# Kernel tuning notes

Measured on AMD Instinct MI355X. Metric: run time of the kernel, lower is better.

Reference implementation:

```python
import jax, jax.numpy as jnp
import numpy as np

N_NODES = 100000
N_EDGES = 3200000
N_GRAPHS = 2000
F_IN, H, N_CLS = 14, 64, 2


def _glorot(key, shape):
    lim = float(np.sqrt(6.0 / (shape[0] + shape[1])))
    return jax.random.uniform(key, shape, jnp.float32, -lim, lim)


def setup_inputs() -> dict:
    key = jax.random.key(0)
    ks = jax.random.split(key, 16)
    x = jax.random.normal(ks[0], (N_NODES, F_IN), jnp.float32)
    edge_index = jax.random.randint(ks[1], (2, N_EDGES), 0, N_NODES, jnp.int64)
    batch = jnp.sort(jax.random.randint(ks[2], (N_NODES,), 0, N_GRAPHS, jnp.int64))
    return {
        "x": x,
        "W1l": _glorot(ks[3], (F_IN, H)), "W1r": _glorot(ks[4], (F_IN, H)), "b1": jnp.zeros((H,), jnp.float32),
        "W2l": _glorot(ks[5], (H, H)), "W2r": _glorot(ks[6], (H, H)), "b2": jnp.zeros((H,), jnp.float32),
        "W3l": _glorot(ks[7], (H, H)), "W3r": _glorot(ks[8], (H, H)), "b3": jnp.zeros((H,), jnp.float32),
        "W4l": _glorot(ks[9], (H, N_CLS)), "W4r": _glorot(ks[10], (H, N_CLS)), "b4": jnp.zeros((N_CLS,), jnp.float32),
        "edge_index": edge_index,
        "batch": batch,
    }


def _sage_conv(x, Wl, Wr, b, src, dst, inv_deg):
    # mean-aggregate neighbor features: messages flow src -> dst (PyG SAGEConv default)
    agg = jax.ops.segment_sum(x[src], dst, num_segments=N_NODES) * inv_deg
    return agg @ Wl + x @ Wr + b


def reference(x, W1l, W1r, b1, W2l, W2r, b2, W3l, W3r, b3, W4l, W4r, b4, edge_index, batch):
    src, dst = edge_index[0], edge_index[1]
    ones = jnp.ones((src.shape[0],), x.dtype)
    deg = jax.ops.segment_sum(ones, dst, num_segments=N_NODES)
    inv_deg = (1.0 / jnp.maximum(deg, 1.0))[:, None]  # [N,1], isolated nodes -> 0 agg

    h = jax.nn.relu(_sage_conv(x, W1l, W1r, b1, src, dst, inv_deg))
    h = jax.nn.relu(_sage_conv(h, W2l, W2r, b2, src, dst, inv_deg))
    h = jax.nn.relu(_sage_conv(h, W3l, W3r, b3, src, dst, inv_deg))
    h = _sage_conv(h, W4l, W4r, b4, src, dst, inv_deg)

    # global_mean_pool over graphs
    gsum = jax.ops.segment_sum(h, batch, num_segments=N_GRAPHS)
    gcnt = jax.ops.segment_sum(jnp.ones((h.shape[0],), h.dtype), batch, num_segments=N_GRAPHS)
    pooled = gsum / jnp.maximum(gcnt, 1.0)[:, None]
    return jax.nn.log_softmax(pooled, axis=-1)
```

## Files before the change

### kernel.cpp

```cpp
#include <hip/hip_runtime.h>
#include <hip/hip_fp16.h>

#define NN 100000
#define NE 3200000
#define NG 2000
#define FIN 14
#define HD 64
#define NC 2

#define NBUK 256
#define BNODES 391
#define P1E 4096
#define BUFCAP 13312

#define AHU 68
#define WCH 136
#define NGB ((NN + 63) / 64)

typedef unsigned int uint;
typedef short short8 __attribute__((ext_vector_type(8)));
typedef float f32x4 __attribute__((ext_vector_type(4)));
union U128 { uint4 u; short8 s; };

__device__ __forceinline__ __half2 u2h(uint u) {
    union { uint u; __half2 h; } c; c.u = u; return c.h;
}
__device__ __forceinline__ uint h2u(__half2 h) {
    union { __half2 h; uint u; } c; c.h = h; return c.u;
}
__device__ __forceinline__ uint pkh(float a, float b) {
    return h2u(__floats2half2_rn(a, b));
}
__device__ __forceinline__ uint pack2bf16(float a, float b) {
    uint ua = __float_as_uint(a), ub = __float_as_uint(b);
    ua = (ua + 0x7FFFu + ((ua >> 16) & 1u)) >> 16;
    ub = (ub + 0x7FFFu + ((ub >> 16) & 1u)) >> 16;
    return ua | (ub << 16);
}
__device__ __forceinline__ unsigned short bf16of(float a) {
    uint ua = __float_as_uint(a);
    return (unsigned short)((ua + 0x7FFFu + ((ua >> 16) & 1u)) >> 16);
}


__global__ __launch_bounds__(256) void k_hist_bucket(const int* __restrict__ dst,
                                                     int* __restrict__ bkcnt) {
    __shared__ int cnt[NBUK];
    int t = threadIdx.x;
    cnt[t] = 0;
    __syncthreads();
    int e0 = blockIdx.x * P1E;
    int m = NE - e0; if (m > P1E) m = P1E;
    for (int e = t; e < m; e += 256) atomicAdd(&cnt[dst[e0 + e] / BNODES], 1);
    __syncthreads();
    if (cnt[t] > 0) atomicAdd(&bkcnt[t], cnt[t]);
}

__global__ void k_scanb(const int* __restrict__ bkcnt, int* __restrict__ bbase,
                        int* __restrict__ bcur) {
    __shared__ int tmp[NBUK];
    int t = threadIdx.x;
    int v = bkcnt[t];
    tmp[t] = v;
    __syncthreads();
    for (int off = 1; off < NBUK; off <<= 1) {
        int u = (t >= off) ? tmp[t - off] : 0;
        __syncthreads();
        tmp[t] += u;
        __syncthreads();
    }
    int excl = tmp[t] - v;
    bbase[t] = excl;
    bcur[t] = excl;
    if (t == NBUK - 1) bbase[NBUK] = tmp[t];
}

__global__ void k_gbounds(const int* __restrict__ batch, int* __restrict__ gstart,
                          int* __restrict__ gend) {
    int i = blockIdx.x * blockDim.x + threadIdx.x;
    if (i < NN) {
        int b = batch[i];
        if (i == 0 || batch[i - 1] != b) gstart[b] = i;
        if (i == NN - 1 || batch[i + 1] != b) gend[b] = i + 1;
    }
}

__global__ __launch_bounds__(256) void k_pass1(
    const int* __restrict__ src, const int* __restrict__ dst,
    int* __restrict__ bcur, int* __restrict__ pairs) {
    __shared__ int cnt[NBUK];
    __shared__ int scanb[NBUK + 1];
    __shared__ int cur[NBUK];
    __shared__ int gbase[NBUK];
    __shared__ int pbuf[P1E];
    __shared__ unsigned char bsl[P1E];
    int t = threadIdx.x;
    int e0 = blockIdx.x * P1E;
    int m = NE - e0; if (m > P1E) m = P1E;
    cnt[t] = 0;
    __syncthreads();
    int ds[16], ss[16], bk[16];
#pragma unroll
    for (int j = 0; j < 16; ++j) {
        int e = t + j * 256;
        if (e < m) {
            ds[j] = dst[e0 + e];
            ss[j] = src[e0 + e];
            bk[j] = ds[j] / BNODES;
            atomicAdd(&cnt[bk[j]], 1);
        } else bk[j] = -1;
    }
    __syncthreads();
    int v = cnt[t];
    scanb[t] = v;
    __syncthreads();
    for (int off = 1; off < 256; off <<= 1) {
        int u = (t >= off) ? scanb[t - off] : 0;
        __syncthreads();
        scanb[t] += u;
        __syncthreads();
    }
    int excl = scanb[t] - v;
    scanb[t] = excl;
    cur[t] = excl;
    if (t == 255) scanb[256] = excl + v;
    __syncthreads();
#pragma unroll
    for (int j = 0; j < 16; ++j) {
        if (bk[j] >= 0) {
            int p = atomicAdd(&cur[bk[j]], 1);
            pbuf[p] = ss[j] | ((ds[j] - bk[j] * BNODES) << 17);
            bsl[p] = (unsigned char)bk[j];
        }
    }
    int cb = scanb[t + 1] - scanb[t];
    if (cb > 0) gbase[t] = atomicAdd(&bcur[t], cb);
    __syncthreads();
    for (int s = t; s < m; s += 256) {
        int b = bsl[s];
        pairs[gbase[b] + (s - scanb[b])] = pbuf[s];
    }
}

__global__ __launch_bounds__(256) void k_pass2(
    const int* __restrict__ pairs, const int* __restrict__ bbase,
    int* __restrict__ deg, int* __restrict__ rs, int* __restrict__ csr) {
    __shared__ int buf1[BUFCAP];
    __shared__ int buf2[BUFCAP];
    __shared__ int cnt[512];
    __shared__ int rsl[512];
    __shared__ int cur[512];
    __shared__ int s1[256];
    int b = blockIdx.x;
    int n0 = b * BNODES;
    if (n0 >= NN) return;
    int nlocal = NN - n0; if (nlocal > BNODES) nlocal = BNODES;
    int t = threadIdx.x;
    int base = bbase[b];
    int m = bbase[b + 1] - base;
    bool fits = (m <= BUFCAP);
    cnt[t] = 0; cnt[t + 256] = 0;
    __syncthreads();
    for (int s = t; s < m; s += 256) {
        int pk = pairs[base + s];
        if (fits) buf1[s] = pk;
        atomicAdd(&cnt[(uint)pk >> 17], 1);
    }
    __syncthreads();
    int c0 = cnt[2 * t], c1 = cnt[2 * t + 1];
    int ps = c0 + c1;
    s1[t] = ps;
    __syncthreads();
    for (int off = 1; off < 256; off <<= 1) {
        int u = (t >= off) ? s1[t - off] : 0;
        __syncthreads();
        s1[t] += u;
        __syncthreads();
    }
    int pexcl = s1[t] - ps;
    rsl[2 * t] = pexcl;          cur[2 * t] = pexcl;
    rsl[2 * t + 1] = pexcl + c0; cur[2 * t + 1] = pexcl + c0;
    __syncthreads();
    for (int i = t; i < nlocal; i += 256) {
        deg[n0 + i] = cnt[i];
        rs[n0 + i] = base + rsl[i];
    }
    if (fits) {
        for (int s = t; s < m; s += 256) {
            int pk = buf1[s];
            int p = atomicAdd(&cur[(uint)pk >> 17], 1);
            buf2[p] = pk & 0x1FFFF;
        }
        __syncthreads();
        for (int s = t; s < m; s += 256) csr[base + s] = buf2[s];
    } else {
        for (int s = t; s < m; s += 256) {
            int pk = pairs[base + s];
            int p = atomicAdd(&cur[(uint)pk >> 17], 1);
            csr[base + p] = pk & 0x1FFFF;
        }
    }
}


__global__ void k_packx(const float* __restrict__ x, uint* __restrict__ xh) {
    int t = blockIdx.x * blockDim.x + threadIdx.x;
    if (t < NN * 8) {
        int row = t >> 3, q = t & 7;
        int j0 = 2 * q, j1 = 2 * q + 1;
        float f0 = (j0 < FIN) ? x[row * FIN + j0] : 0.f;
        float f1 = (j1 < FIN) ? x[row * FIN + j1] : 0.f;
        xh[t] = pkh(f0, f1);
    }
}


__global__ __launch_bounds__(256, 6) void k_layer1(
    const float* __restrict__ x, const uint* __restrict__ xh, uint* __restrict__ hout,
    const float* __restrict__ Wl, const float* __restrict__ Wr, const float* __restrict__ b,
    const int* __restrict__ rs, const int* __restrict__ deg, const int* __restrict__ csr) {
    __shared__ float2 sW[FIN][HD];
    __shared__ float sb[HD];
    __shared__ float2 sAH[4][16];
    for (int i = threadIdx.x; i < FIN * HD; i += 256) {
        int k = i >> 6, j = i & 63;
        sW[k][j] = make_float2(Wl[i], Wr[i]);
    }
    if (threadIdx.x < HD) sb[threadIdx.x] = b[threadIdx.x];
    __syncthreads();
    int lane = threadIdx.x & 63, wid = threadIdx.x >> 6;
    int sub = lane >> 3;
    int fq = lane & 7;
    int ngroups = (NN + 3) / 4;
    for (int g = blockIdx.x; g < ngroups; g += gridDim.x) {
        int n = g * 4 + wid;
        bool act = n < NN;
        if (act) {
            int s0 = rs[n], d = deg[n];
            float xv = (lane < FIN) ? x[n * FIN + lane] : 0.f;
            __half2 Z = __float2half2_rn(0.f);
            __half2 A0 = Z, A1 = Z, A2 = Z, A3 = Z, A4 = Z, A5 = Z, A6 = Z, A7 = Z;
            for (int base = 0; base < d; base += 64) {
                int rem = d - base; if (rem > 64) rem = 64;
                int idxv = (lane < rem) ? csr[s0 + base + lane] : 0;
                int j = 0;
                for (; j + 64 <= rem; j += 64) {
                    int i0 = __shfl(idxv, j + 0 + sub);
                    int i1 = __shfl(idxv, j + 8 + sub);
                    int i2 = __shfl(idxv, j + 16 + sub);
                    int i3 = __shfl(idxv, j + 24 + sub);
                    int i4 = __shfl(idxv, j + 32 + sub);
                    int i5 = __shfl(idxv, j + 40 + sub);
                    int i6 = __shfl(idxv, j + 48 + sub);
                    int i7 = __shfl(idxv, j + 56 + sub);
                    A0 = __hadd2(A0, u2h(xh[(size_t)i0 * 8 + fq]));
                    A1 = __hadd2(A1, u2h(xh[(size_t)i1 * 8 + fq]));
                    A2 = __hadd2(A2, u2h(xh[(size_t)i2 * 8 + fq]));
                    A3 = __hadd2(A3, u2h(xh[(size_t)i3 * 8 + fq]));
                    A4 = __hadd2(A4, u2h(xh[(size_t)i4 * 8 + fq]));
                    A5 = __hadd2(A5, u2h(xh[(size_t)i5 * 8 + fq]));
                    A6 = __hadd2(A6, u2h(xh[(size_t)i6 * 8 + fq]));
                    A7 = __hadd2(A7, u2h(xh[(size_t)i7 * 8 + fq]));
                }
                for (; j + 8 <= rem; j += 8) {
                    int i0 = __shfl(idxv, j + sub);
                    A0 = __hadd2(A0, u2h(xh[(size_t)i0 * 8 + fq]));
                }
                if (j < rem) {
                    int i0 = __shfl(idxv, j + sub);
                    if (sub < rem - j) A0 = __hadd2(A0, u2h(xh[(size_t)i0 * 8 + fq]));
                }
            }
            A0 = __hadd2(A0, A1); A2 = __hadd2(A2, A3);
            A4 = __hadd2(A4, A5); A6 = __hadd2(A6, A7);
            A0 = __hadd2(A0, A2); A4 = __hadd2(A4, A6);
            A0 = __hadd2(A0, A4);
            float ax = __low2float(A0), ay = __high2float(A0);
            for (int off = 8; off <= 32; off <<= 1) {
                ax += __shfl_xor(ax, off);
                ay += __shfl_xor(ay, off);
            }
            float inv = 1.0f / (float)(d > 1 ? d : 1);
            float e0 = __shfl(ax, lane >> 1);
            float e1 = __shfl(ay, lane >> 1);
            float sel = (lane & 1) ? e1 : e0;
            if (lane < 16) sAH[wid][lane] = make_float2((lane < FIN) ? sel * inv : 0.f, xv);
        }
        float out = sb[lane];
#pragma unroll
        for (int k = 0; k < FIN; ++k) {
            float2 w = sW[k][lane];
            float2 ah = sAH[wid][k];
            out += ah.x * w.x + ah.y * w.y;
        }
        out = fmaxf(out, 0.f);
        float o2 = __shfl_xor(out, 1);
        if (act && !(lane & 1)) hout[(size_t)n * 32 + (lane >> 1)] = pkh(out, o2);
    }
}


template <bool FUSEZ>
__global__ __launch_bounds__(256, 4) void k_layerH(
    const uint* __restrict__ hin, uint* __restrict__ hout,
    const float* __restrict__ Wl, const float* __restrict__ Wr, const float* __restrict__ b,
    const float* __restrict__ W4l, float* __restrict__ z,
    const int* __restrict__ rs, const int* __restrict__ deg, const int* __restrict__ csr) {
    __shared__ uint sAHb[4][16 * AHU];
    __shared__ unsigned short sWT[64 * WCH];
    __shared__ float sb[HD], sW4l[HD * NC];
    for (int i = threadIdx.x; i < 64 * 128; i += 256) {
        int j = i >> 7, kk = i & 127;
        float v = (kk < 64) ? Wl[kk * 64 + j] : Wr[(kk - 64) * 64 + j];
        sWT[j * WCH + kk] = bf16of(v);
    }
    if (threadIdx.x < HD) sb[threadIdx.x] = b[threadIdx.x];
    if (FUSEZ && threadIdx.x < HD * NC) sW4l[threadIdx.x] = W4l[threadIdx.x];
    __syncthreads();
    int lane = threadIdx.x & 63, wid = threadIdx.x >> 6;
    uint* AH = sAHb[wid];
    int sub = lane >> 4;
    int fq = lane & 15;
    const uint2* hb2 = (const uint2*)hin;
    int n0 = (blockIdx.x * 4 + wid) * 16;
    for (int i = 0; i < 16; ++i) {
        int n = n0 + i;
        if (n < NN) {
            int s0 = rs[n], d = deg[n];
            __half2 Zh = __float2half2_rn(0.f);
            __half2 P0 = Zh, P1 = Zh, P2 = Zh, P3 = Zh, P4 = Zh, P5 = Zh, P6 = Zh, P7 = Zh;
            __half2 Q0 = Zh, Q1 = Zh, Q2 = Zh, Q3 = Zh, Q4 = Zh, Q5 = Zh, Q6 = Zh, Q7 = Zh;
            for (int base = 0; base < d; base += 64) {
                int rem = d - base; if (rem > 64) rem = 64;
                int idxv = (lane < rem) ? csr[s0 + base + lane] : 0;
                int j = 0;
                for (; j + 32 <= rem; j += 32) {
                    int i0 = __shfl(idxv, j + 0 + sub);
                    int i1 = __shfl(idxv, j + 4 + sub);
                    int i2 = __shfl(idxv, j + 8 + sub);
                    int i3 = __shfl(idxv, j + 12 + sub);
                    int i4 = __shfl(idxv, j + 16 + sub);
                    int i5 = __shfl(idxv, j + 20 + sub);
                    int i6 = __shfl(idxv, j + 24 + sub);
                    int i7 = __shfl(idxv, j + 28 + sub);
                    uint2 U;
                    U = hb2[(size_t)i0 * 16 + fq]; P0 = __hadd2(P0, u2h(U.x)); Q0 = __hadd2(Q0, u2h(U.y));
                    U = hb2[(size_t)i1 * 16 + fq]; P1 = __hadd2(P1, u2h(U.x)); Q1 = __hadd2(Q1, u2h(U.y));
                    U = hb2[(size_t)i2 * 16 + fq]; P2 = __hadd2(P2, u2h(U.x)); Q2 = __hadd2(Q2, u2h(U.y));
                    U = hb2[(size_t)i3 * 16 + fq]; P3 = __hadd2(P3, u2h(U.x)); Q3 = __hadd2(Q3, u2h(U.y));
                    U = hb2[(size_t)i4 * 16 + fq]; P4 = __hadd2(P4, u2h(U.x)); Q4 = __hadd2(Q4, u2h(U.y));
                    U = hb2[(size_t)i5 * 16 + fq]; P5 = __hadd2(P5, u2h(U.x)); Q5 = __hadd2(Q5, u2h(U.y));
                    U = hb2[(size_t)i6 * 16 + fq]; P6 = __hadd2(P6, u2h(U.x)); Q6 = __hadd2(Q6, u2h(U.y));
                    U = hb2[(size_t)i7 * 16 + fq]; P7 = __hadd2(P7, u2h(U.x)); Q7 = __hadd2(Q7, u2h(U.y));
                }
                for (; j + 4 <= rem; j += 4) {
                    int i0 = __shfl(idxv, j + sub);
                    uint2 U = hb2[(size_t)i0 * 16 + fq];
                    P0 = __hadd2(P0, u2h(U.x)); Q0 = __hadd2(Q0, u2h(U.y));
                }
                if (j < rem) {
                    int i0 = __shfl(idxv, j + sub);
                    if (sub < rem - j) {
                        uint2 U = hb2[(size_t)i0 * 16 + fq];
                        P0 = __hadd2(P0, u2h(U.x)); Q0 = __hadd2(Q0, u2h(U.y));
                    }
                }
            }
            P0 = __hadd2(P0, P1); P2 = __hadd2(P2, P3);
            P4 = __hadd2(P4, P5); P6 = __hadd2(P6, P7);
            Q0 = __hadd2(Q0, Q1); Q2 = __hadd2(Q2, Q3);
            Q4 = __hadd2(Q4, Q5); Q6 = __hadd2(Q6, Q7);
            P0 = __hadd2(P0, P2); P4 = __hadd2(P4, P6);
            Q0 = __hadd2(Q0, Q2); Q4 = __hadd2(Q4, Q6);
            P0 = __hadd2(P0, P4); Q0 = __hadd2(Q0, Q4);
            float ax = __low2float(P0), ay = __high2float(P0);
            float az = __low2float(Q0), aw = __high2float(Q0);
            for (int off = 16; off <= 32; off <<= 1) {
                ax += __shfl_xor(ax, off);
                ay += __shfl_xor(ay, off);
                az += __shfl_xor(az, off);
                aw += __shfl_xor(aw, off);
            }
            float inv = 1.0f / (float)(d > 1 ? d : 1);
            ax *= inv; ay *= inv; az *= inv; aw *= inv;
            if (lane < 16) {
                AH[i * AHU + 2 * fq] = pack2bf16(ax, ay);
                AH[i * AHU + 2 * fq + 1] = pack2bf16(az, aw);
            }
            if (lane < 32) {
                __half2 hh = u2h(hin[(size_t)n * 32 + lane]);
                AH[i * AHU + 32 + lane] = pack2bf16(__low2float(hh), __high2float(hh));
            }
        } else {
            if (lane < 32) { AH[i * AHU + lane] = 0; AH[i * AHU + 32 + lane] = 0; }
        }
    }
    int r16 = lane & 15, qg = lane >> 4;
    short8 afr[4];
#pragma unroll
    for (int c = 0; c < 4; ++c) {
        U128 a;
        a.u = *(const uint4*)&AH[r16 * AHU + 16 * c + 4 * qg];
        afr[c] = a.s;
    }
    f32x4 acc[4];
#pragma unroll
    for (int t = 0; t < 4; ++t) {
        float bv = sb[16 * t + r16];
        acc[t] = (f32x4){bv, bv, bv, bv};
    }
#pragma unroll
    for (int t = 0; t < 4; ++t) {
#pragma unroll
        for (int c = 0; c < 4; ++c) {
            U128 bf;
            bf.u = *(const uint4*)(sWT + (16 * t + r16) * WCH + 32 * c + 8 * qg);
            acc[t] = __builtin_amdgcn_mfma_f32_16x16x32_bf16(afr[c], bf.s, acc[t], 0, 0, 0);
        }
    }
    float rz0[4] = {0.f, 0.f, 0.f, 0.f}, rz1[4] = {0.f, 0.f, 0.f, 0.f};
#pragma unroll
    for (int t = 0; t < 4; ++t) {
        float wz0 = 0.f, wz1 = 0.f;
        if (FUSEZ) {
            wz0 = sW4l[(16 * t + r16) * NC + 0];
            wz1 = sW4l[(16 * t + r16) * NC + 1];
        }
#pragma unroll
        for (int r = 0; r < 4; ++r) {
            int m = n0 + qg * 4 + r;
            float out = fmaxf(acc[t][r], 0.f);
            float o2 = __shfl_xor(out, 1);
            if (!(lane & 1) && m < NN)
                hout[(size_t)m * 32 + 8 * t + (r16 >> 1)] = pkh(out, o2);
            if (FUSEZ) { rz0[r] += out * wz0; rz1[r] += out * wz1; }
        }
    }
    if (FUSEZ) {
#pragma unroll
        for (int r = 0; r < 4; ++r) {
            float a0 = rz0[r], a1 = rz1[r];
            for (int off = 1; off < 16; off <<= 1) {
                a0 += __shfl_xor(a0, off);
                a1 += __shfl_xor(a1, off);
            }
            int m = n0 + qg * 4 + r;
            if (r16 == 0 && m < NN) ((float2*)z)[m] = make_float2(a0, a1);
        }
    }
}


__global__ __launch_bounds__(256) void k_pool(
    const uint* __restrict__ h3, const float* __restrict__ z,
    const float* __restrict__ W4r, const float* __restrict__ b4,
    const int* __restrict__ rs, const int* __restrict__ deg, const int* __restrict__ csr,
    const int* __restrict__ batch, float* __restrict__ gsum) {
    __shared__ float sW[HD * NC];
    if (threadIdx.x < HD * NC) sW[threadIdx.x] = W4r[threadIdx.x];
    __syncthreads();
    const float2* z2 = (const float2*)z;
    int lane = threadIdx.x & 63, wid = threadIdx.x >> 6;
    int stride = gridDim.x * 4;
    for (int n = blockIdx.x * 4 + wid; n < NN; n += stride) {
        float r0 = 0.f, r1 = 0.f;
        if (lane < 32) {
            __half2 h = u2h(h3[(size_t)n * 32 + lane]);
            float f0 = __low2float(h), f1 = __high2float(h);
            r0 = f0 * sW[(2 * lane) * NC + 0] + f1 * sW[(2 * lane + 1) * NC + 0];
            r1 = f0 * sW[(2 * lane) * NC + 1] + f1 * sW[(2 * lane + 1) * NC + 1];
        }
        int s0 = rs[n], d = deg[n];
        float a0 = 0.f, a1 = 0.f;
        for (int j = lane; j < d; j += 64) {
            int s = csr[s0 + j];
            float2 zv = z2[s];
            a0 += zv.x;
            a1 += zv.y;
        }
        for (int off = 32; off; off >>= 1) {
            r0 += __shfl_xor(r0, off);
            r1 += __shfl_xor(r1, off);
            a0 += __shfl_xor(a0, off);
            a1 += __shfl_xor(a1, off);
        }
        if (lane == 0) {
            float inv = 1.0f / (float)(d > 1 ? d : 1);
            float o0 = a0 * inv + r0 + b4[0];
            float o1 = a1 * inv + r1 + b4[1];
            int gg = batch[n];
            atomicAdd(&gsum[gg * 2 + 0], o0);
            atomicAdd(&gsum[gg * 2 + 1], o1);
        }
    }
}

__global__ void k_final(const float* __restrict__ gsum, const int* __restrict__ gstart,
                        const int* __restrict__ gend, float* __restrict__ out) {
    int g = blockIdx.x * blockDim.x + threadIdx.x;
    if (g < NG) {
        int cnt = gend[g] - gstart[g];
        float inv = 1.0f / (float)(cnt > 1 ? cnt : 1);
        float p0 = gsum[g * 2 + 0] * inv;
        float p1 = gsum[g * 2 + 1] * inv;
        float m = fmaxf(p0, p1);
        float lse = m + logf(expf(p0 - m) + expf(p1 - m));
        out[g * 2 + 0] = p0 - lse;
        out[g * 2 + 1] = p1 - lse;
    }
}


extern "C" void kernel_launch(void* const* d_in, const int* in_sizes, int n_in,
                              void* d_out, int out_size, void* d_ws, size_t ws_size,
                              hipStream_t stream) {
    const float* x   = (const float*)d_in[0];
    const float* W1l = (const float*)d_in[1];
    const float* W1r = (const float*)d_in[2];
    const float* b1  = (const float*)d_in[3];
    const float* W2l = (const float*)d_in[4];
    const float* W2r = (const float*)d_in[5];
    const float* b2  = (const float*)d_in[6];
    const float* W3l = (const float*)d_in[7];
    const float* W3r = (const float*)d_in[8];
    const float* b3  = (const float*)d_in[9];
    const float* W4l = (const float*)d_in[10];
    const float* W4r = (const float*)d_in[11];
    const float* b4  = (const float*)d_in[12];
    const int* ei    = (const int*)d_in[13];
    const int* batch = (const int*)d_in[14];
    const int* src = ei;
    const int* dst = ei + NE;
    float* out = (float*)d_out;

    char* w = (char*)d_ws;
    int* deg    = (int*)w; w += (size_t)NN * 4;
    int* rs     = (int*)w; w += (size_t)NN * 4;
    int* csr    = (int*)w; w += (size_t)NE * 4;
    int* gstart = (int*)w; w += (size_t)NG * 4;
    int* gend   = (int*)w; w += (size_t)NG * 4;
    int* bkcnt  = (int*)w; w += NBUK * 4;
    int* bbase  = (int*)w; w += (NBUK + 1) * 4;
    int* bcur   = (int*)w; w += NBUK * 4;
    w = (char*)(((uintptr_t)w + 255) & ~(uintptr_t)255);
    uint* xh    = (uint*)w; w += (size_t)NN * 8 * 4;
    uint* hA    = (uint*)w; w += (size_t)NN * 32 * 4;
    uint* hB    = (uint*)w; w += (size_t)NN * 32 * 4;
    float* z    = (float*)w; w += (size_t)NN * NC * 4;
    float* gsum = (float*)w; w += (size_t)NG * NC * 4;
    int* pairs = (int*)hB;

    const int P1B = (NE + P1E - 1) / P1E;

    hipMemsetAsync(bkcnt, 0, NBUK * 4, stream);
    hipMemsetAsync(gstart, 0, (size_t)NG * 4, stream);
    hipMemsetAsync(gend, 0, (size_t)NG * 4, stream);
    hipMemsetAsync(gsum, 0, (size_t)NG * NC * 4, stream);

    k_hist_bucket<<<P1B, 256, 0, stream>>>(dst, bkcnt);
    k_packx<<<(NN * 8 + 255) / 256, 256, 0, stream>>>(x, xh);
    k_gbounds<<<(NN + 255) / 256, 256, 0, stream>>>(batch, gstart, gend);
    k_scanb<<<1, NBUK, 0, stream>>>(bkcnt, bbase, bcur);
    k_pass1<<<P1B, 256, 0, stream>>>(src, dst, bcur, pairs);
    k_pass2<<<NBUK, 256, 0, stream>>>(pairs, bbase, deg, rs, csr);

    k_layer1<<<1536, 256, 0, stream>>>(x, xh, hA, W1l, W1r, b1, rs, deg, csr);
    k_layerH<false><<<NGB, 256, 0, stream>>>(hA, hB, W2l, W2r, b2, nullptr, nullptr, rs, deg, csr);
    k_layerH<true><<<NGB, 256, 0, stream>>>(hB, hA, W3l, W3r, b3, W4l, z, rs, deg, csr);
    k_pool<<<2048, 256, 0, stream>>>(hA, z, W4r, b4, rs, deg, csr, batch, gsum);
    k_final<<<(NG + 255) / 256, 256, 0, stream>>>(gsum, gstart, gend, out);
}
```

Measured before the change: 525.7 us.

## Shrink layerH tiles to 16 nodes per block with register-resident weight fragments

Restructures the hidden-layer kernel so each block handles 16 nodes (4 per wave) and each wave computes one 16-column slice of the output with a single MFMA chain. Weight fragments are loaded straight from global memory into registers instead of staging a transposed bf16 weight tile in LDS, and the shared aggregation tile uses an XOR swizzle in place of padding. The aim is to cut LDS use, raise occupancy and spread gather work over more blocks, at the cost of reloading weights per block (about 4x more blocks) and an extra block-wide barrier plus an LDS reduction for the fused z output.

```diff
diff --git a/kernel.cpp b/kernel.cpp
--- a/kernel.cpp
+++ b/kernel.cpp
@@ -13,10 +13,6 @@
 #define P1E 4096
 #define BUFCAP 13312
 
-#define AHU 68
-#define WCH 136
-#define NGB ((NN + 63) / 64)
-
 typedef unsigned int uint;
 typedef short short8 __attribute__((ext_vector_type(8)));
 typedef float f32x4 __attribute__((ext_vector_type(4)));
@@ -37,9 +33,9 @@
     ub = (ub + 0x7FFFu + ((ub >> 16) & 1u)) >> 16;
     return ua | (ub << 16);
 }
-__device__ __forceinline__ unsigned short bf16of(float a) {
+__device__ __forceinline__ short bf16of(float a) {
     uint ua = __float_as_uint(a);
-    return (unsigned short)((ua + 0x7FFFu + ((ua >> 16) & 1u)) >> 16);
+    return (short)((ua + 0x7FFFu + ((ua >> 16) & 1u)) >> 16);
 }
 
 
@@ -306,25 +302,32 @@
     const float* __restrict__ Wl, const float* __restrict__ Wr, const float* __restrict__ b,
     const float* __restrict__ W4l, float* __restrict__ z,
     const int* __restrict__ rs, const int* __restrict__ deg, const int* __restrict__ csr) {
-    __shared__ uint sAHb[4][16 * AHU];
-    __shared__ unsigned short sWT[64 * WCH];
-    __shared__ float sb[HD], sW4l[HD * NC];
-    for (int i = threadIdx.x; i < 64 * 128; i += 256) {
-        int j = i >> 7, kk = i & 127;
-        float v = (kk < 64) ? Wl[kk * 64 + j] : Wr[(kk - 64) * 64 + j];
-        sWT[j * WCH + kk] = bf16of(v);
-    }
-    if (threadIdx.x < HD) sb[threadIdx.x] = b[threadIdx.x];
-    if (FUSEZ && threadIdx.x < HD * NC) sW4l[threadIdx.x] = W4l[threadIdx.x];
-    __syncthreads();
+    __shared__ uint AH[16 * 64];
+    __shared__ float zb[4][16][2];
     int lane = threadIdx.x & 63, wid = threadIdx.x >> 6;
-    uint* AH = sAHb[wid];
+    int r16 = lane & 15, qg = lane >> 4;
+    int jj = 16 * wid + r16;
+    short8 bfr[4];
+#pragma unroll
+    for (int c = 0; c < 4; ++c) {
+#pragma unroll
+        for (int i = 0; i < 8; ++i) {
+            int k = 32 * c + 8 * qg + i;
+            float v = (k < 64) ? Wl[k * 64 + jj] : Wr[(k - 64) * 64 + jj];
+            bfr[c][i] = bf16of(v);
+        }
+    }
+    float bv = b[jj];
+    float wz0 = 0.f, wz1 = 0.f;
+    if (FUSEZ) { wz0 = W4l[jj * NC + 0]; wz1 = W4l[jj * NC + 1]; }
     int sub = lane >> 4;
     int fq = lane & 15;
     const uint2* hb2 = (const uint2*)hin;
-    int n0 = (blockIdx.x * 4 + wid) * 16;
-    for (int i = 0; i < 16; ++i) {
-        int n = n0 + i;
+    int n0 = blockIdx.x * 16;
+    for (int i = 0; i < 4; ++i) {
+        int irow = wid * 4 + i;
+        int n = n0 + irow;
+        int swz = (irow & 7) << 2;
         if (n < NN) {
             int s0 = rs[n], d = deg[n];
             __half2 Zh = __float2half2_rn(0.f);
@@ -384,57 +387,34 @@
             float inv = 1.0f / (float)(d > 1 ? d : 1);
             ax *= inv; ay *= inv; az *= inv; aw *= inv;
             if (lane < 16) {
-                AH[i * AHU + 2 * fq] = pack2bf16(ax, ay);
-                AH[i * AHU + 2 * fq + 1] = pack2bf16(az, aw);
+                uint2* p = (uint2*)&AH[irow * 64 + ((2 * fq) ^ swz)];
+                *p = make_uint2(pack2bf16(ax, ay), pack2bf16(az, aw));
             }
             if (lane < 32) {
                 __half2 hh = u2h(hin[(size_t)n * 32 + lane]);
-                AH[i * AHU + 32 + lane] = pack2bf16(__low2float(hh), __high2float(hh));
+                AH[irow * 64 + ((32 + lane) ^ swz)] = pack2bf16(__low2float(hh), __high2float(hh));
             }
         } else {
-            if (lane < 32) { AH[i * AHU + lane] = 0; AH[i * AHU + 32 + lane] = 0; }
-        }
-    }
-    int r16 = lane & 15, qg = lane >> 4;
-    short8 afr[4];
+            AH[irow * 64 + lane] = 0;
+        }
+    }
+    __syncthreads();
+    f32x4 acc = (f32x4){bv, bv, bv, bv};
 #pragma unroll
     for (int c = 0; c < 4; ++c) {
         U128 a;
-        a.u = *(const uint4*)&AH[r16 * AHU + 16 * c + 4 * qg];
-        afr[c] = a.s;
-    }
-    f32x4 acc[4];
-#pragma unroll
-    for (int t = 0; t < 4; ++t) {
-        float bv = sb[16 * t + r16];
-        acc[t] = (f32x4){bv, bv, bv, bv};
-    }
-#pragma unroll
-    for (int t = 0; t < 4; ++t) {
-#pragma unroll
-        for (int c = 0; c < 4; ++c) {
-            U128 bf;
-            bf.u = *(const uint4*)(sWT + (16 * t + r16) * WCH + 32 * c + 8 * qg);
-            acc[t] = __builtin_amdgcn_mfma_f32_16x16x32_bf16(afr[c], bf.s, acc[t], 0, 0, 0);
-        }
-    }
-    float rz0[4] = {0.f, 0.f, 0.f, 0.f}, rz1[4] = {0.f, 0.f, 0.f, 0.f};
-#pragma unroll
-    for (int t = 0; t < 4; ++t) {
-        float wz0 = 0.f, wz1 = 0.f;
-        if (FUSEZ) {
-            wz0 = sW4l[(16 * t + r16) * NC + 0];
-            wz1 = sW4l[(16 * t + r16) * NC + 1];
-        }
-#pragma unroll
-        for (int r = 0; r < 4; ++r) {
-            int m = n0 + qg * 4 + r;
-            float out = fmaxf(acc[t][r], 0.f);
-            float o2 = __shfl_xor(out, 1);
-            if (!(lane & 1) && m < NN)
-                hout[(size_t)m * 32 + 8 * t + (r16 >> 1)] = pkh(out, o2);
-            if (FUSEZ) { rz0[r] += out * wz0; rz1[r] += out * wz1; }
-        }
+        a.u = *(const uint4*)&AH[r16 * 64 + ((16 * c + 4 * qg) ^ ((r16 & 7) << 2))];
+        acc = __builtin_amdgcn_mfma_f32_16x16x32_bf16(a.s, bfr[c], acc, 0, 0, 0);
+    }
+    float rz0[4], rz1[4];
+#pragma unroll
+    for (int r = 0; r < 4; ++r) {
+        int m = n0 + qg * 4 + r;
+        float out = fmaxf(acc[r], 0.f);
+        float o2 = __shfl_xor(out, 1);
+        if (!(lane & 1) && m < NN)
+            hout[(size_t)m * 32 + 8 * wid + (r16 >> 1)] = pkh(out, o2);
+        if (FUSEZ) { rz0[r] = out * wz0; rz1[r] = out * wz1; }
     }
     if (FUSEZ) {
 #pragma unroll
@@ -444,8 +424,14 @@
                 a0 += __shfl_xor(a0, off);
                 a1 += __shfl_xor(a1, off);
             }
-            int m = n0 + qg * 4 + r;
-            if (r16 == 0 && m < NN) ((float2*)z)[m] = make_float2(a0, a1);
+            if (r16 == 0) { zb[wid][qg * 4 + r][0] = a0; zb[wid][qg * 4 + r][1] = a1; }
+        }
+        __syncthreads();
+        int t = threadIdx.x;
+        if (t < 16 && n0 + t < NN) {
+            float a0 = zb[0][t][0] + zb[1][t][0] + zb[2][t][0] + zb[3][t][0];
+            float a1 = zb[0][t][1] + zb[1][t][1] + zb[2][t][1] + zb[3][t][1];
+            ((float2*)z)[n0 + t] = make_float2(a0, a1);
         }
     }
 }
@@ -551,6 +537,7 @@
     int* pairs = (int*)hB;
 
     const int P1B = (NE + P1E - 1) / P1E;
+    const int HGB = (NN + 15) / 16;
 
     hipMemsetAsync(bkcnt, 0, NBUK * 4, stream);
     hipMemsetAsync(gstart, 0, (size_t)NG * 4, stream);
@@ -565,8 +552,8 @@
     k_pass2<<<NBUK, 256, 0, stream>>>(pairs, bbase, deg, rs, csr);
 
     k_layer1<<<1536, 256, 0, stream>>>(x, xh, hA, W1l, W1r, b1, rs, deg, csr);
-    k_layerH<false><<<NGB, 256, 0, stream>>>(hA, hB, W2l, W2r, b2, nullptr, nullptr, rs, deg, csr);
-    k_layerH<true><<<NGB, 256, 0, stream>>>(hB, hA, W3l, W3r, b3, W4l, z, rs, deg, csr);
+    k_layerH<false><<<HGB, 256, 0, stream>>>(hA, hB, W2l, W2r, b2, nullptr, nullptr, rs, deg, csr);
+    k_layerH<true><<<HGB, 256, 0, stream>>>(hB, hA, W3l, W3r, b3, W4l, z, rs, deg, csr);
     k_pool<<<2048, 256, 0, stream>>>(hA, z, W4r, b4, rs, deg, csr, batch, gsum);
     k_final<<<(NG + 255) / 256, 256, 0, stream>>>(gsum, gstart, gend, out);
 }
```

Result: faster. 424.3 us (-19.3%).
